# Optimization experiments

Measured on AMD Instinct MI355X. Metric: run time of the kernel, lower is better.

The kernel has to match this reference:

```python
import jax, jax.numpy as jnp
import numpy as np

NEG_INF = -9e15  # matches torch's -9000000000000000.0 mask value
ALPHA = 0.2      # LeakyReLU negative slope


def setup_inputs() -> dict:
    key = jax.random.key(0)
    k1, k2, k3, k4 = jax.random.split(key, 4)
    B, N, Fin, Fout, H = 32, 512, 256, 64, 8
    x = jax.random.normal(k1, (B, N, Fin), dtype=jnp.float32)
    adj = (jax.random.uniform(k2, (B, N, N)) < 0.5).astype(jnp.float32)
    # W: Linear(in_features, out_features*n_heads, bias=False) weight, stored as (Fin, Fout*H)
    W = jax.random.normal(k3, (Fin, Fout * H), dtype=jnp.float32) / np.sqrt(Fin).astype(np.float32)
    # a: attention vector per head over concat(src,dst) features -> (H, 2*Fout)
    a = jax.random.normal(k4, (H, 2 * Fout), dtype=jnp.float32) * 0.1
    return {"x": x, "adj": adj, "W": W, "a": a}


def reference(x, adj, W, a):
    # x: (B,N,Fin), adj: (B,N,N), W: (Fin, H*F), a: (H, 2F)
    B, N, _ = x.shape
    H, twoF = a.shape
    F = twoF // 2
    h = (x @ W).reshape(B, N, H, F)  # (B,N,H,F)
    # Decompose concat-score: e_ij = lrelu(h_i . a_src + h_j . a_dst) -- same math
    # as (cat(h_i,h_j) * a).sum(-1) without materializing (B,N,N,H,2F).
    s_src = jnp.einsum('bnhf,hf->bnh', h, a[:, :F])  # (B,N,H)
    s_dst = jnp.einsum('bnhf,hf->bnh', h, a[:, F:])  # (B,N,H)
    e = s_src[:, :, None, :] + s_dst[:, None, :, :]  # (B,N,N,H)
    e = jax.nn.leaky_relu(e, negative_slope=ALPHA)
    e = jnp.where(adj[..., None] > 0, e, NEG_INF)
    attn = jax.nn.softmax(e, axis=2)  # softmax over neighbors j (dim=2)
    # dropout omitted (eval mode / p effectively 0 for the reference baseline)
    h_prime = jnp.einsum('bijh,bjhf->bihf', attn, h)  # (B,N,H,F)
    return h_prime.reshape(B, N, H * F)  # concat=True
```

## Files before the change

kernel.cpp:

```cpp
#include <hip/hip_runtime.h>
#include <hip/hip_bf16.h>


#define ALPHA 0.2f

typedef __bf16 bf16x8 __attribute__((ext_vector_type(8)));
typedef __bf16 bf16x4 __attribute__((ext_vector_type(4)));
typedef float  f32x4  __attribute__((ext_vector_type(4)));

#define HT_STRIDE 520
#define WT_STRIDE 264

struct Smem {
    __bf16 hT[64][HT_STRIDE];
    __bf16 WT[64][WT_STRIDE];
    float  ssrc[512], sdst[512], rsum[512];
    float  asrc[64], adst[64];
};

__device__ inline bf16x8 ld8(const __bf16* p) { return *(const bf16x8*)p; }
__device__ inline bf16x8 ld8(const float* p) {
    float4 a0 = *(const float4*)p;
    float4 a1 = *(const float4*)(p + 4);
    bf16x8 r;
    r[0]=(__bf16)a0.x; r[1]=(__bf16)a0.y; r[2]=(__bf16)a0.z; r[3]=(__bf16)a0.w;
    r[4]=(__bf16)a1.x; r[5]=(__bf16)a1.y; r[6]=(__bf16)a1.z; r[7]=(__bf16)a1.w;
    return r;
}
__device__ inline void ld8f(const __bf16* p, float* o) {
    bf16x8 v = *(const bf16x8*)p;
    #pragma unroll
    for (int u = 0; u < 8; ++u) o[u] = (float)v[u];
}
__device__ inline void ld8f(const float* p, float* o) {
    float4 a0 = *(const float4*)p;
    float4 a1 = *(const float4*)(p + 4);
    o[0]=a0.x; o[1]=a0.y; o[2]=a0.z; o[3]=a0.w;
    o[4]=a1.x; o[5]=a1.y; o[6]=a1.z; o[7]=a1.w;
}

template <typename T>
__device__ void gat_body(const T* __restrict__ x, const T* __restrict__ adj,
                         const T* __restrict__ W, const T* __restrict__ a,
                         float* __restrict__ out, Smem& sm,
                         int b, int h, int tid) {
    const int wave = tid >> 6, lane = tid & 63;
    const int quad = lane >> 4, col = lane & 15;

    if (tid < 128) {
        float v = (float)a[h * 128 + tid];
        if (tid < 64) sm.asrc[tid] = v; else sm.adst[tid - 64] = v;
    }
    {
        int c = tid & 63, k0 = tid >> 6;
        #pragma unroll 4
        for (int t = 0; t < 32; ++t) {
            int k = k0 + t * 8;
            sm.WT[c][k] = (__bf16)(float)W[(long)k * 512 + h * 64 + c];
        }
    }
    __syncthreads();

    {
        const T* xb = x + (long)b * 512 * 256;
        f32x4 acc[4][4] = {};
        for (int ks = 0; ks < 8; ++ks) {
            int k0 = ks * 32 + quad * 8;
            bf16x8 av[4], bv[4];
            #pragma unroll
            for (int it = 0; it < 4; ++it)
                av[it] = ld8(xb + (long)(wave * 64 + it * 16 + col) * 256 + k0);
            #pragma unroll
            for (int nt = 0; nt < 4; ++nt)
                bv[nt] = *(const bf16x8*)(&sm.WT[nt * 16 + col][k0]);
            #pragma unroll
            for (int it = 0; it < 4; ++it)
                #pragma unroll
                for (int nt = 0; nt < 4; ++nt)
                    acc[it][nt] = __builtin_amdgcn_mfma_f32_16x16x32_bf16(av[it], bv[nt], acc[it][nt], 0, 0, 0);
        }
        #pragma unroll
        for (int it = 0; it < 4; ++it)
            #pragma unroll
            for (int nt = 0; nt < 4; ++nt) {
                int f = nt * 16 + col;
                int j = wave * 64 + it * 16 + quad * 4;
                bf16x4 pk = { (__bf16)acc[it][nt][0], (__bf16)acc[it][nt][1],
                              (__bf16)acc[it][nt][2], (__bf16)acc[it][nt][3] };
                *(bf16x4*)(&sm.hT[f][j]) = pk;
            }
    }
    __syncthreads();

    {
        float as = 0.f, ad = 0.f;
        #pragma unroll 8
        for (int f = 0; f < 64; ++f) {
            float v = (float)sm.hT[f][tid];
            as += v * sm.asrc[f];
            ad += v * sm.adst[f];
        }
        sm.ssrc[tid] = as;
        sm.sdst[tid] = ad;
    }
    __syncthreads();

    {
        float si[4], sacc[4] = {0.f, 0.f, 0.f, 0.f};
        const T* arow[4];
        #pragma unroll
        for (int it = 0; it < 4; ++it) {
            int i = wave * 64 + it * 16 + col;
            si[it]   = sm.ssrc[i];
            arow[it] = adj + ((long)(b * 512 + i)) * 512;
        }
        f32x4 acc[4][4] = {};
        for (int ks = 0; ks < 16; ++ks) {
            int j0 = ks * 32 + quad * 8;
            f32x4 s0 = *(const f32x4*)&sm.sdst[j0];
            f32x4 s1 = *(const f32x4*)&sm.sdst[j0 + 4];
            float sd[8] = {s0[0],s0[1],s0[2],s0[3],s1[0],s1[1],s1[2],s1[3]};
            bf16x8 P[4];
            #pragma unroll
            for (int it = 0; it < 4; ++it) {
                float am[8];
                ld8f(arow[it] + j0, am);
                #pragma unroll
                for (int u = 0; u < 8; ++u) {
                    float e = si[it] + sd[u];
                    e = e > 0.f ? e : ALPHA * e;
                    float p = (am[u] > 0.f) ? __expf(e) : 0.f;
                    __bf16 pb = (__bf16)p;
                    sacc[it] += (float)pb;
                    P[it][u] = pb;
                }
            }
            #pragma unroll
            for (int nt = 0; nt < 4; ++nt) {
                bf16x8 bv = *(const bf16x8*)(&sm.hT[nt * 16 + col][j0]);
                #pragma unroll
                for (int it = 0; it < 4; ++it)
                    acc[it][nt] = __builtin_amdgcn_mfma_f32_16x16x32_bf16(P[it], bv, acc[it][nt], 0, 0, 0);
            }
        }
        #pragma unroll
        for (int it = 0; it < 4; ++it) {
            float s = sacc[it];
            s += __shfl_xor(s, 16);
            s += __shfl_xor(s, 32);
            if (quad == 0) sm.rsum[wave * 64 + it * 16 + col] = s;
        }
        __syncthreads();
        #pragma unroll
        for (int it = 0; it < 4; ++it)
            #pragma unroll
            for (int r = 0; r < 4; ++r) {
                int i = wave * 64 + it * 16 + quad * 4 + r;
                float s = sm.rsum[i];
                float inv = (s > 0.f) ? 1.0f / s : 0.f;
                float* orow = out + ((long)(b * 512 + i)) * 512 + h * 64;
                #pragma unroll
                for (int nt = 0; nt < 4; ++nt)
                    orow[nt * 16 + col] = acc[it][nt][r] * inv;
            }
    }
}

__global__ void k_probe(const unsigned int* __restrict__ adjw,
                        int* __restrict__ flag) {
    unsigned int v = adjw[threadIdx.x];
    unsigned long long m = __ballot((v & 0xFFFFu) == 0x3F80u);
    if (threadIdx.x == 0) flag[0] = (m != 0ull) ? 1 : 0;
}

__global__ __launch_bounds__(512, 1) void k_gat(const void* __restrict__ x,
                                                const void* __restrict__ adj,
                                                const void* __restrict__ W,
                                                const void* __restrict__ a,
                                                float* __restrict__ out,
                                                const int* __restrict__ flag) {
    __shared__ Smem sm;
    const int h = blockIdx.x, b = blockIdx.y, tid = threadIdx.x;
    if (*flag)
        gat_body<__bf16>((const __bf16*)x, (const __bf16*)adj,
                         (const __bf16*)W, (const __bf16*)a, out, sm, b, h, tid);
    else
        gat_body<float>((const float*)x, (const float*)adj,
                        (const float*)W, (const float*)a, out, sm, b, h, tid);
}

extern "C" void kernel_launch(void* const* d_in, const int* in_sizes, int n_in,
                              void* d_out, int out_size, void* d_ws, size_t ws_size,
                              hipStream_t stream) {
    const void* x   = d_in[0];
    const void* adj = d_in[1];
    const void* W   = d_in[2];
    const void* a   = d_in[3];
    float* out = (float*)d_out;
    int* flag = (int*)d_ws;

    k_probe<<<1, 64, 0, stream>>>((const unsigned int*)adj, flag);
    k_gat<<<dim3(8, 32), 512, 0, stream>>>(x, adj, W, a, out, flag);
}
```

Before: 152.2 us.

## Split query rows across two blocks, stream W in chunks, drop dtype probe

Measured after the change: 161.0 us. 5.8% more time.

```diff
diff --git a/kernel.cpp b/kernel.cpp
--- a/kernel.cpp
+++ b/kernel.cpp
@@ -9,16 +9,16 @@
 typedef float  f32x4  __attribute__((ext_vector_type(4)));
 
 #define HT_STRIDE 520
-#define WT_STRIDE 264
+#define WT_STRIDE 40
 
 struct Smem {
     __bf16 hT[64][HT_STRIDE];
     __bf16 WT[64][WT_STRIDE];
-    float  ssrc[512], sdst[512], rsum[512];
+    float  ssrc[512], sdst[512];
+    float  rsum[256];
     float  asrc[64], adst[64];
 };
 
-__device__ inline bf16x8 ld8(const __bf16* p) { return *(const bf16x8*)p; }
 __device__ inline bf16x8 ld8(const float* p) {
     float4 a0 = *(const float4*)p;
     float4 a1 = *(const float4*)(p + 4);
@@ -27,57 +27,45 @@
     r[4]=(__bf16)a1.x; r[5]=(__bf16)a1.y; r[6]=(__bf16)a1.z; r[7]=(__bf16)a1.w;
     return r;
 }
-__device__ inline void ld8f(const __bf16* p, float* o) {
-    bf16x8 v = *(const bf16x8*)p;
-    #pragma unroll
-    for (int u = 0; u < 8; ++u) o[u] = (float)v[u];
-}
-__device__ inline void ld8f(const float* p, float* o) {
-    float4 a0 = *(const float4*)p;
-    float4 a1 = *(const float4*)(p + 4);
-    o[0]=a0.x; o[1]=a0.y; o[2]=a0.z; o[3]=a0.w;
-    o[4]=a1.x; o[5]=a1.y; o[6]=a1.z; o[7]=a1.w;
-}
 
-template <typename T>
-__device__ void gat_body(const T* __restrict__ x, const T* __restrict__ adj,
-                         const T* __restrict__ W, const T* __restrict__ a,
-                         float* __restrict__ out, Smem& sm,
-                         int b, int h, int tid) {
+__global__ __launch_bounds__(512, 4) void k_gat(const float* __restrict__ x,
+                                                const float* __restrict__ adj,
+                                                const float* __restrict__ W,
+                                                const float* __restrict__ a,
+                                                float* __restrict__ out) {
+    __shared__ Smem sm;
+    const int ihalf = blockIdx.x, h = blockIdx.y, b = blockIdx.z;
+    const int tid  = threadIdx.x;
     const int wave = tid >> 6, lane = tid & 63;
     const int quad = lane >> 4, col = lane & 15;
 
     if (tid < 128) {
-        float v = (float)a[h * 128 + tid];
+        float v = a[h * 128 + tid];
         if (tid < 64) sm.asrc[tid] = v; else sm.adst[tid - 64] = v;
     }
-    {
-        int c = tid & 63, k0 = tid >> 6;
-        #pragma unroll 4
-        for (int t = 0; t < 32; ++t) {
-            int k = k0 + t * 8;
-            sm.WT[c][k] = (__bf16)(float)W[(long)k * 512 + h * 64 + c];
-        }
-    }
-    __syncthreads();
 
     {
-        const T* xb = x + (long)b * 512 * 256;
+        const float* xb = x + (long)b * 512 * 256;
         f32x4 acc[4][4] = {};
+        const int c = tid & 63, kl = tid >> 6;
         for (int ks = 0; ks < 8; ++ks) {
-            int k0 = ks * 32 + quad * 8;
+            #pragma unroll
+            for (int t = 0; t < 4; ++t)
+                sm.WT[c][kl + t * 8] = (__bf16)W[(long)(ks * 32 + kl + t * 8) * 512 + h * 64 + c];
+            __syncthreads();
             bf16x8 av[4], bv[4];
             #pragma unroll
             for (int it = 0; it < 4; ++it)
-                av[it] = ld8(xb + (long)(wave * 64 + it * 16 + col) * 256 + k0);
+                av[it] = ld8(xb + (long)(wave * 64 + it * 16 + col) * 256 + ks * 32 + quad * 8);
             #pragma unroll
             for (int nt = 0; nt < 4; ++nt)
-                bv[nt] = *(const bf16x8*)(&sm.WT[nt * 16 + col][k0]);
+                bv[nt] = *(const bf16x8*)(&sm.WT[nt * 16 + col][quad * 8]);
             #pragma unroll
             for (int it = 0; it < 4; ++it)
                 #pragma unroll
                 for (int nt = 0; nt < 4; ++nt)
                     acc[it][nt] = __builtin_amdgcn_mfma_f32_16x16x32_bf16(av[it], bv[nt], acc[it][nt], 0, 0, 0);
+            __syncthreads();
         }
         #pragma unroll
         for (int it = 0; it < 4; ++it)
@@ -106,25 +94,26 @@
     __syncthreads();
 
     {
-        float si[4], sacc[4] = {0.f, 0.f, 0.f, 0.f};
-        const T* arow[4];
+        float si[2], sacc[2] = {0.f, 0.f};
+        const float* arow[2];
         #pragma unroll
-        for (int it = 0; it < 4; ++it) {
-            int i = wave * 64 + it * 16 + col;
-            si[it]   = sm.ssrc[i];
+        for (int it = 0; it < 2; ++it) {
+            int i = ihalf * 256 + wave * 32 + it * 16 + col;
+            si[it]   = sm.ssrc[i & 511];
             arow[it] = adj + ((long)(b * 512 + i)) * 512;
         }
-        f32x4 acc[4][4] = {};
+        f32x4 acc[2][4] = {};
         for (int ks = 0; ks < 16; ++ks) {
             int j0 = ks * 32 + quad * 8;
             f32x4 s0 = *(const f32x4*)&sm.sdst[j0];
             f32x4 s1 = *(const f32x4*)&sm.sdst[j0 + 4];
             float sd[8] = {s0[0],s0[1],s0[2],s0[3],s1[0],s1[1],s1[2],s1[3]};
-            bf16x8 P[4];
+            bf16x8 P[2];
             #pragma unroll
-            for (int it = 0; it < 4; ++it) {
-                float am[8];
-                ld8f(arow[it] + j0, am);
+            for (int it = 0; it < 2; ++it) {
+                float4 a0 = *(const float4*)(arow[it] + j0);
+                float4 a1 = *(const float4*)(arow[it] + j0 + 4);
+                float am[8] = {a0.x,a0.y,a0.z,a0.w,a1.x,a1.y,a1.z,a1.w};
                 #pragma unroll
                 for (int u = 0; u < 8; ++u) {
                     float e = si[it] + sd[u];
@@ -139,24 +128,25 @@
             for (int nt = 0; nt < 4; ++nt) {
                 bf16x8 bv = *(const bf16x8*)(&sm.hT[nt * 16 + col][j0]);
                 #pragma unroll
-                for (int it = 0; it < 4; ++it)
+                for (int it = 0; it < 2; ++it)
                     acc[it][nt] = __builtin_amdgcn_mfma_f32_16x16x32_bf16(P[it], bv, acc[it][nt], 0, 0, 0);
             }
         }
         #pragma unroll
-        for (int it = 0; it < 4; ++it) {
+        for (int it = 0; it < 2; ++it) {
             float s = sacc[it];
             s += __shfl_xor(s, 16);
             s += __shfl_xor(s, 32);
-            if (quad == 0) sm.rsum[wave * 64 + it * 16 + col] = s;
+            if (quad == 0) sm.rsum[wave * 32 + it * 16 + col] = s;
         }
         __syncthreads();
         #pragma unroll
-        for (int it = 0; it < 4; ++it)
+        for (int it = 0; it < 2; ++it)
             #pragma unroll
             for (int r = 0; r < 4; ++r) {
-                int i = wave * 64 + it * 16 + quad * 4 + r;
-                float s = sm.rsum[i];
+                int li = wave * 32 + it * 16 + quad * 4 + r;
+                int i  = ihalf * 256 + li;
+                float s = sm.rsum[li];
                 float inv = (s > 0.f) ? 1.0f / s : 0.f;
                 float* orow = out + ((long)(b * 512 + i)) * 512 + h * 64;
                 #pragma unroll
@@ -166,39 +156,15 @@
     }
 }
 
-__global__ void k_probe(const unsigned int* __restrict__ adjw,
-                        int* __restrict__ flag) {
-    unsigned int v = adjw[threadIdx.x];
-    unsigned long long m = __ballot((v & 0xFFFFu) == 0x3F80u);
-    if (threadIdx.x == 0) flag[0] = (m != 0ull) ? 1 : 0;
-}
-
-__global__ __launch_bounds__(512, 1) void k_gat(const void* __restrict__ x,
-                                                const void* __restrict__ adj,
-                                                const void* __restrict__ W,
-                                                const void* __restrict__ a,
-                                                float* __restrict__ out,
-                                                const int* __restrict__ flag) {
-    __shared__ Smem sm;
-    const int h = blockIdx.x, b = blockIdx.y, tid = threadIdx.x;
-    if (*flag)
-        gat_body<__bf16>((const __bf16*)x, (const __bf16*)adj,
-                         (const __bf16*)W, (const __bf16*)a, out, sm, b, h, tid);
-    else
-        gat_body<float>((const float*)x, (const float*)adj,
-                        (const float*)W, (const float*)a, out, sm, b, h, tid);
-}
-
 extern "C" void kernel_launch(void* const* d_in, const int* in_sizes, int n_in,
                               void* d_out, int out_size, void* d_ws, size_t ws_size,
                               hipStream_t stream) {
-    const void* x   = d_in[0];
-    const void* adj = d_in[1];
-    const void* W   = d_in[2];
-    const void* a   = d_in[3];
+    const float* x   = (const float*)d_in[0];
+    const float* adj = (const float*)d_in[1];
+    const float* W   = (const float*)d_in[2];
+    const float* a   = (const float*)d_in[3];
     float* out = (float*)d_out;
-    int* flag = (int*)d_ws;
+    (void)d_ws; (void)ws_size;
 
-    k_probe<<<1, 64, 0, stream>>>((const unsigned int*)adj, flag);
-    k_gat<<<dim3(8, 32), 512, 0, stream>>>(x, adj, W, a, out, flag);
+    k_gat<<<dim3(2, 8, 32), 512, 0, stream>>>(x, adj, W, a, out);
 }
```
